# Kernel optimization log

Measured on AMD Instinct MI355X. Metric: run time of the kernel, lower is better.

Reference implementation:

```python
import jax, jax.numpy as jnp
import numpy as np

B, N, E = 32, 2048, 768
OUT = 384
SPARSITY = 4
LOCAL_C = (E + SPARSITY - 1) // SPARSITY  # 192
HID = 16
LN_EPS = 1e-5


def _layernorm(x, w, b):
    mu = jnp.mean(x, axis=-1, keepdims=True)
    var = jnp.mean(jnp.square(x - mu), axis=-1, keepdims=True)
    return (x - mu) * jax.lax.rsqrt(var + LN_EPS) * w + b


def setup_inputs() -> dict:
    key = jax.random.key(0)
    ks = jax.random.split(key, 8)
    s = 0.02
    return {
        "x": jax.random.normal(ks[0], (B, N, E), dtype=jnp.float32),
        # global head: Linear(E,16) -> LN(16) -> GELU -> Linear(16,1)
        "w_g1": jax.random.normal(ks[1], (E, HID), dtype=jnp.float32) * s,
        "b_g1": jnp.zeros((HID,), dtype=jnp.float32),
        "ln_g_w": jnp.ones((HID,), dtype=jnp.float32),
        "ln_g_b": jnp.zeros((HID,), dtype=jnp.float32),
        "w_g2": jax.random.normal(ks[2], (HID, 1), dtype=jnp.float32) * s,
        "b_g2": jnp.zeros((1,), dtype=jnp.float32),
        # local head: Linear(192,384) -> LN(384) -> GELU
        "w_l": jax.random.normal(ks[3], (LOCAL_C, OUT), dtype=jnp.float32) * s,
        "b_l": jnp.zeros((OUT,), dtype=jnp.float32),
        "ln_l_w": jnp.ones((OUT,), dtype=jnp.float32),
        "ln_l_b": jnp.zeros((OUT,), dtype=jnp.float32),
    }


def reference(x, w_g1, b_g1, ln_g_w, ln_g_b, w_g2, b_g2, w_l, b_l, ln_l_w, ln_l_b):
    # local branch: strided gather -> Linear -> LN -> GELU  [B,N,OUT]
    local = x[..., ::SPARSITY]                                   # [B,N,192]
    local_feat = jax.nn.gelu(_layernorm(local @ w_l + b_l, ln_l_w, ln_l_b),
                             approximate=False)
    # global branch: Linear -> LN -> GELU -> Linear -> [B,N,1] (broadcasts)
    g = jax.nn.gelu(_layernorm(x @ w_g1 + b_g1, ln_g_w, ln_g_b),
                    approximate=False)
    global_feat = g @ w_g2 + b_g2                                # [B,N,1]
    # AdaptiveAvgPool1d(OUT) on last dim; E % OUT == 0 -> exact pairwise mean
    pooled = jnp.mean(x.reshape(B, N, OUT, E // OUT), axis=-1)   # [B,N,OUT]
    return global_feat + pooled + local_feat
```

## Files before the change

kernel.cpp:

```cpp
#include <hip/hip_runtime.h>
#include <hip/hip_bf16.h>

#define B_   32
#define N_   2048
#define E_   768
#define OUT_ 384
#define HID_ 16
constexpr int ROWS   = B_ * N_;
constexpr int TILE_M = 32;
constexpr int NT     = OUT_ / 16;
constexpr int KT_L   = 6;
constexpr int KT_G   = 24;
constexpr int S_AL   = 194;
constexpr int S_PL   = 392;

typedef __attribute__((ext_vector_type(8))) short bf16x8;
typedef __attribute__((ext_vector_type(4))) float f32x4;

__device__ __forceinline__ short f2bf(float f) {
  __hip_bfloat16 h = __float2bfloat16(f);
  return __builtin_bit_cast(short, h);
}
__device__ __forceinline__ float bf2f(short s) {
  union { unsigned u; float f; } v; v.u = ((unsigned)(unsigned short)s) << 16;
  return v.f;
}

__device__ __forceinline__ void gload_pair(f32x4& d0, f32x4& d1, const float* a) {
  asm volatile("global_load_dwordx4 %0, %2, off\n\t"
               "global_load_dwordx4 %1, %2, off offset:16"
               : "=&v"(d0), "=&v"(d1)
               : "v"(a));
}
__device__ __forceinline__ void gload_frag(bf16x8& d, const short* a) {
  asm volatile("global_load_dwordx4 %0, %1, off" : "=&v"(d) : "v"(a));
}
#define WAITV(n) do { asm volatile("s_waitcnt vmcnt(" #n ")" ::: "memory"); \
                      __builtin_amdgcn_sched_barrier(0); } while (0)
#define RAWBAR() do { __builtin_amdgcn_sched_barrier(0);                     \
                      asm volatile("s_waitcnt lgkmcnt(0)" ::: "memory");     \
                      __builtin_amdgcn_s_barrier();                          \
                      __builtin_amdgcn_sched_barrier(0); } while (0)

__device__ __forceinline__ float fast_erf(float x) {
  const float ax = __builtin_fabsf(x);
  const float t  = __builtin_amdgcn_rcpf(__builtin_fmaf(0.47047f, ax, 1.0f));
  float p = __builtin_fmaf(0.7478556f, t, -0.0958798f);
  p = __builtin_fmaf(p, t, 0.3480242f);
  const float e = __expf(-ax * ax);
  const float y = __builtin_fmaf(-p * t, e, 1.0f);
  return __builtin_copysignf(y, x);
}
__device__ __forceinline__ float gelu(float v) {
  return 0.5f * v * (1.0f + fast_erf(v * 0.70710678118654752f));
}

__global__ void prep_kernel(const float* __restrict__ w_l, const float* __restrict__ w_g1,
                            short* __restrict__ wsL, short* __restrict__ wsG) {
  int t = blockIdx.x * blockDim.x + threadIdx.x;
  int wave = t >> 6, ln = t & 63;
  int kg = ln >> 4, c16 = ln & 15;
  if (wave < NT * KT_L) {
    int n = wave / KT_L, ks = wave % KT_L;
    bf16x8 v;
#pragma unroll
    for (int j = 0; j < 8; ++j) {
      int k = ks * 32 + kg * 8 + j;
      v[j] = f2bf(w_l[k * OUT_ + n * 16 + c16]);
    }
    *reinterpret_cast<bf16x8*>(&wsL[(size_t)(wave * 64 + ln) * 8]) = v;
  } else if (wave < NT * KT_L + KT_G) {
    int ks = wave - NT * KT_L;
    bf16x8 v;
#pragma unroll
    for (int j = 0; j < 8; ++j) {
      int k = ks * 32 + kg * 8 + j;
      v[j] = f2bf(w_g1[k * HID_ + c16]);
    }
    *reinterpret_cast<bf16x8*>(&wsG[(size_t)(ks * 64 + ln) * 8]) = v;
  }
}

template <bool USE_WS>
__global__ __launch_bounds__(256, 2)
void spectre_kernel(const float* __restrict__ x,
                    const float* __restrict__ w_g1, const float* __restrict__ b_g1,
                    const float* __restrict__ ln_g_w, const float* __restrict__ ln_g_b,
                    const float* __restrict__ w_g2, const float* __restrict__ b_g2,
                    const float* __restrict__ w_l, const float* __restrict__ b_l,
                    const float* __restrict__ ln_l_w, const float* __restrict__ ln_l_b,
                    const short* __restrict__ wsL, const short* __restrict__ wsG,
                    float* __restrict__ out) {
  __shared__ short al[TILE_M * S_AL];
  __shared__ short pl[TILE_M * S_PL];
  __shared__ float red2[4][16][17];
  __shared__ float reds[4][32][2];
  __shared__ float gfl[32];

  const int tid = threadIdx.x;
  const int wv  = tid >> 6;
  const int wvp = wv >> 1;
  const int wvk = wv & 1;
  const int ln  = tid & 63;
  const int kg  = ln >> 4;
  const int l15 = ln & 15;
  const int row0 = blockIdx.x * TILE_M;

  const float* xb = x + (size_t)(row0 + wvp * 16) * E_;

  const float bg  = b_g1[l15];
  const float lgw = ln_g_w[l15];
  const float lgb = ln_g_b[l15];
  const float wg2 = w_g2[l15];
  const float bg2 = b_g2[0];
  float blv[6], lwv[6], lbv[6];
#pragma unroll
  for (int j = 0; j < 6; ++j) {
    const int col = (wv * 6 + j) * 16 + l15;
    blv[j] = b_l[col];
    lwv[j] = ln_l_w[col];
    lbv[j] = ln_l_b[col];
  }
  const short* wlp = USE_WS ? (wsL + ((size_t)(wv * 6) * KT_L * 64 + ln) * 8) : nullptr;

  f32x4 accg = {0.f, 0.f, 0.f, 0.f};
  const int alr = (wvp * 16 + l15);
  if constexpr (USE_WS) {
    asm volatile("s_waitcnt vmcnt(0)" ::: "memory");
    __builtin_amdgcn_sched_barrier(0);

    bf16x8 gbv[12];
    const short* wgp = wsG + ((size_t)(wvk * 12) * 64 + ln) * 8;
#pragma unroll
    for (int i = 0; i < 12; ++i) gload_frag(gbv[i], wgp + i * 512);

    f32x4 xa0[6], xa1[6], xb0[6], xb1[6];
    const float* pA = xb + l15 * E_ + kg * 8;
#pragma unroll
    for (int i = 0; i < 6; ++i) gload_pair(xa0[i], xa1[i], pA + (wvk * 12 + i) * 32);
#pragma unroll
    for (int i = 0; i < 6; ++i) gload_pair(xb0[i], xb1[i], pA + (wvk * 12 + 6 + i) * 32);

    WAITV(12);
#pragma unroll
    for (int i = 0; i < 6; ++i) {
      const int ks = wvk * 12 + i;
      const f32x4 u0 = xa0[i], u1 = xa1[i];
      short2 lv;
      lv.x = f2bf(u0[0]);
      lv.y = f2bf(u1[0]);
      *reinterpret_cast<short2*>(&al[alr * S_AL + 8 * ks + 2 * kg]) = lv;
      short4 pv;
      pv.x = f2bf(0.5f * (u0[0] + u0[1]));
      pv.y = f2bf(0.5f * (u0[2] + u0[3]));
      pv.z = f2bf(0.5f * (u1[0] + u1[1]));
      pv.w = f2bf(0.5f * (u1[2] + u1[3]));
      *reinterpret_cast<short4*>(&pl[alr * S_PL + ks * 16 + kg * 4]) = pv;
      const bf16x8 a = { lv.x, f2bf(u0[1]), f2bf(u0[2]), f2bf(u0[3]),
                         lv.y, f2bf(u1[1]), f2bf(u1[2]), f2bf(u1[3]) };
      accg = __builtin_amdgcn_mfma_f32_16x16x32_bf16(a, gbv[i], accg, 0, 0, 0);
    }
    WAITV(0);
#pragma unroll
    for (int i = 0; i < 6; ++i) {
      const int ks = wvk * 12 + 6 + i;
      const f32x4 u0 = xb0[i], u1 = xb1[i];
      short2 lv;
      lv.x = f2bf(u0[0]);
      lv.y = f2bf(u1[0]);
      *reinterpret_cast<short2*>(&al[alr * S_AL + 8 * ks + 2 * kg]) = lv;
      short4 pv;
      pv.x = f2bf(0.5f * (u0[0] + u0[1]));
      pv.y = f2bf(0.5f * (u0[2] + u0[3]));
      pv.z = f2bf(0.5f * (u1[0] + u1[1]));
      pv.w = f2bf(0.5f * (u1[2] + u1[3]));
      *reinterpret_cast<short4*>(&pl[alr * S_PL + ks * 16 + kg * 4]) = pv;
      const bf16x8 a = { lv.x, f2bf(u0[1]), f2bf(u0[2]), f2bf(u0[3]),
                         lv.y, f2bf(u1[1]), f2bf(u1[2]), f2bf(u1[3]) };
      accg = __builtin_amdgcn_mfma_f32_16x16x32_bf16(a, gbv[6 + i], accg, 0, 0, 0);
    }
    __builtin_amdgcn_sched_barrier(0);
  } else {
    const float* pA = xb + l15 * E_ + kg * 8;
#pragma unroll
    for (int i = 0; i < 12; ++i) {
      const int ks = wvk * 12 + i;
      const float4 u0 = *reinterpret_cast<const float4*>(pA + ks * 32);
      const float4 u1 = *reinterpret_cast<const float4*>(pA + ks * 32 + 4);
      short2 lv;
      lv.x = f2bf(u0.x);
      lv.y = f2bf(u1.x);
      *reinterpret_cast<short2*>(&al[alr * S_AL + 8 * ks + 2 * kg]) = lv;
      short4 pv;
      pv.x = f2bf(0.5f * (u0.x + u0.y));
      pv.y = f2bf(0.5f * (u0.z + u0.w));
      pv.z = f2bf(0.5f * (u1.x + u1.y));
      pv.w = f2bf(0.5f * (u1.z + u1.w));
      *reinterpret_cast<short4*>(&pl[alr * S_PL + ks * 16 + kg * 4]) = pv;
      bf16x8 b;
#pragma unroll
      for (int j = 0; j < 8; ++j) b[j] = f2bf(w_g1[(ks * 32 + kg * 8 + j) * HID_ + l15]);
      const bf16x8 a = { lv.x, f2bf(u0.y), f2bf(u0.z), f2bf(u0.w),
                         lv.y, f2bf(u1.y), f2bf(u1.z), f2bf(u1.w) };
      accg = __builtin_amdgcn_mfma_f32_16x16x32_bf16(a, b, accg, 0, 0, 0);
    }
  }
#pragma unroll
  for (int r = 0; r < 4; ++r) red2[wv][kg * 4 + r][l15] = accg[r];

  bf16x8 fA[6], fB[6];
  if constexpr (USE_WS) {
#pragma unroll
    for (int j = 0; j < 6; ++j) gload_frag(fA[j], wlp + (j * 6 + 0) * 512);
#pragma unroll
    for (int j = 0; j < 6; ++j) gload_frag(fB[j], wlp + (j * 6 + 1) * 512);
    RAWBAR();
  } else {
    __syncthreads();
  }

  f32x4 acc0[6], acc1[6];
#pragma unroll
  for (int j = 0; j < 6; ++j) {
    acc0[j] = (f32x4){0.f, 0.f, 0.f, 0.f};
    acc1[j] = (f32x4){0.f, 0.f, 0.f, 0.f};
  }

  if constexpr (USE_WS) {
    float gf[4];
#pragma unroll
    for (int r = 0; r < 4; ++r) {
      const int row = kg * 4 + r;
      const float y = red2[2 * wvp][row][l15] + red2[2 * wvp + 1][row][l15] + bg;
      float s = y, q = y * y;
#pragma unroll
      for (int m = 1; m < 16; m <<= 1) {
        s += __shfl_xor(s, m);
        q += __shfl_xor(q, m);
      }
      const float mean = s * (1.f / 16.f);
      const float var  = q * (1.f / 16.f) - mean * mean;
      const float rstd = rsqrtf(var + 1e-5f);
      const float vn = (y - mean) * rstd * lgw + lgb;
      float ps = gelu(vn) * wg2;
#pragma unroll
      for (int m = 1; m < 16; m <<= 1) ps += __shfl_xor(ps, m);
      gf[r] = ps + bg2;
    }
    if (wvk == 0 && l15 == 0) {
#pragma unroll
      for (int r = 0; r < 4; ++r) gfl[wvp * 16 + kg * 4 + r] = gf[r];
    }

#define LKSTEP(KS, FREG, NEXTKS, NEXTREG, LASTWAIT)                                   \
    do {                                                                              \
      WAITV(LASTWAIT);                                                                \
      const bf16x8 aL0 = *reinterpret_cast<const bf16x8*>(                            \
          &al[l15 * S_AL + (KS) * 32 + kg * 8]);                                      \
      const bf16x8 aL1 = *reinterpret_cast<const bf16x8*>(                            \
          &al[(16 + l15) * S_AL + (KS) * 32 + kg * 8]);                               \
      __builtin_amdgcn_s_setprio(1);                                                  \
      _Pragma("unroll")                                                               \
      for (int j = 0; j < 6; ++j) {                                                   \
        acc0[j] = __builtin_amdgcn_mfma_f32_16x16x32_bf16(aL0, FREG[j], acc0[j], 0, 0, 0); \
        acc1[j] = __builtin_amdgcn_mfma_f32_16x16x32_bf16(aL1, FREG[j], acc1[j], 0, 0, 0); \
      }                                                                               \
      __builtin_amdgcn_s_setprio(0);                                                  \
      if ((NEXTKS) < KT_L) {                                                          \
        _Pragma("unroll")                                                             \
        for (int j = 0; j < 6; ++j)                                                   \
          gload_frag(NEXTREG[j], wlp + (j * 6 + (NEXTKS)) * 512);                     \
      }                                                                               \
    } while (0)

    LKSTEP(0, fA, 2, fA, 6);
    LKSTEP(1, fB, 3, fB, 6);
    LKSTEP(2, fA, 4, fA, 6);
    LKSTEP(3, fB, 5, fB, 6);
    LKSTEP(4, fA, 6, fA, 6);
    LKSTEP(5, fB, 6, fB, 0);
#undef LKSTEP
    __builtin_amdgcn_sched_barrier(0);
  } else {
    float gf[4];
#pragma unroll
    for (int r = 0; r < 4; ++r) {
      const int row = kg * 4 + r;
      const float y = red2[2 * wvp][row][l15] + red2[2 * wvp + 1][row][l15] + bg;
      float s = y, q = y * y;
#pragma unroll
      for (int m = 1; m < 16; m <<= 1) { s += __shfl_xor(s, m); q += __shfl_xor(q, m); }
      const float mean = s * (1.f / 16.f);
      const float var  = q * (1.f / 16.f) - mean * mean;
      const float rstd = rsqrtf(var + 1e-5f);
      const float vn = (y - mean) * rstd * lgw + lgb;
      float ps = gelu(vn) * wg2;
#pragma unroll
      for (int m = 1; m < 16; m <<= 1) ps += __shfl_xor(ps, m);
      gf[r] = ps + bg2;
    }
    if (wvk == 0 && l15 == 0) {
#pragma unroll
      for (int r = 0; r < 4; ++r) gfl[wvp * 16 + kg * 4 + r] = gf[r];
    }
#pragma unroll
    for (int ks = 0; ks < KT_L; ++ks) {
      const bf16x8 aL0 = *reinterpret_cast<const bf16x8*>(&al[l15 * S_AL + ks * 32 + kg * 8]);
      const bf16x8 aL1 = *reinterpret_cast<const bf16x8*>(&al[(16 + l15) * S_AL + ks * 32 + kg * 8]);
#pragma unroll
      for (int j = 0; j < 6; ++j) {
        const int ng = wv * 6 + j;
        bf16x8 b;
#pragma unroll
        for (int jj = 0; jj < 8; ++jj)
          b[jj] = f2bf(w_l[(ks * 32 + kg * 8 + jj) * OUT_ + ng * 16 + l15]);
        acc0[j] = __builtin_amdgcn_mfma_f32_16x16x32_bf16(aL0, b, acc0[j], 0, 0, 0);
        acc1[j] = __builtin_amdgcn_mfma_f32_16x16x32_bf16(aL1, b, acc1[j], 0, 0, 0);
      }
    }
  }

  float s10[4] = {0.f, 0.f, 0.f, 0.f}, s20[4] = {0.f, 0.f, 0.f, 0.f};
  float s11[4] = {0.f, 0.f, 0.f, 0.f}, s21[4] = {0.f, 0.f, 0.f, 0.f};
#pragma unroll
  for (int j = 0; j < 6; ++j) {
#pragma unroll
    for (int r = 0; r < 4; ++r) {
      const float v0 = acc0[j][r] + blv[j];
      acc0[j][r] = v0;
      s10[r] += v0; s20[r] += v0 * v0;
      const float v1 = acc1[j][r] + blv[j];
      acc1[j][r] = v1;
      s11[r] += v1; s21[r] += v1 * v1;
    }
  }
#pragma unroll
  for (int m = 1; m < 16; m <<= 1) {
#pragma unroll
    for (int r = 0; r < 4; ++r) {
      s10[r] += __shfl_xor(s10[r], m);
      s20[r] += __shfl_xor(s20[r], m);
      s11[r] += __shfl_xor(s11[r], m);
      s21[r] += __shfl_xor(s21[r], m);
    }
  }
  if (l15 == 0) {
#pragma unroll
    for (int r = 0; r < 4; ++r) {
      reds[wv][kg * 4 + r][0] = s10[r];
      reds[wv][kg * 4 + r][1] = s20[r];
      reds[wv][16 + kg * 4 + r][0] = s11[r];
      reds[wv][16 + kg * 4 + r][1] = s21[r];
    }
  }
  if constexpr (USE_WS) {
    RAWBAR();
  } else {
    __syncthreads();
  }

  float mean0[4], rstd0[4], mean1[4], rstd1[4];
#pragma unroll
  for (int r = 0; r < 4; ++r) {
    const int row = kg * 4 + r;
    float t1 = reds[0][row][0] + reds[1][row][0] + reds[2][row][0] + reds[3][row][0];
    float t2 = reds[0][row][1] + reds[1][row][1] + reds[2][row][1] + reds[3][row][1];
    mean0[r] = t1 * (1.f / 384.f);
    rstd0[r] = rsqrtf(t2 * (1.f / 384.f) - mean0[r] * mean0[r] + 1e-5f);
    t1 = reds[0][16 + row][0] + reds[1][16 + row][0] + reds[2][16 + row][0] + reds[3][16 + row][0];
    t2 = reds[0][16 + row][1] + reds[1][16 + row][1] + reds[2][16 + row][1] + reds[3][16 + row][1];
    mean1[r] = t1 * (1.f / 384.f);
    rstd1[r] = rsqrtf(t2 * (1.f / 384.f) - mean1[r] * mean1[r] + 1e-5f);
  }
#pragma unroll
  for (int n = 0; n < 6; ++n) {
    const int col = (wv * 6 + n) * 16 + l15;
#pragma unroll
    for (int r = 0; r < 4; ++r) {
      const int rowA = kg * 4 + r;
      {
        const float pooled = bf2f(pl[rowA * S_PL + col]);
        const float vn = (acc0[n][r] - mean0[r]) * rstd0[r] * lwv[n] + lbv[n];
        out[(size_t)(row0 + rowA) * OUT_ + col] = gelu(vn) + gfl[rowA] + pooled;
      }
      {
        const int rowB = 16 + rowA;
        const float pooled = bf2f(pl[rowB * S_PL + col]);
        const float vn = (acc1[n][r] - mean1[r]) * rstd1[r] * lwv[n] + lbv[n];
        out[(size_t)(row0 + rowB) * OUT_ + col] = gelu(vn) + gfl[rowB] + pooled;
      }
    }
  }
}

extern "C" void kernel_launch(void* const* d_in, const int* in_sizes, int n_in,
                              void* d_out, int out_size, void* d_ws, size_t ws_size,
                              hipStream_t stream) {
  (void)in_sizes; (void)n_in; (void)out_size;
  const float* x      = (const float*)d_in[0];
  const float* w_g1   = (const float*)d_in[1];
  const float* b_g1   = (const float*)d_in[2];
  const float* ln_g_w = (const float*)d_in[3];
  const float* ln_g_b = (const float*)d_in[4];
  const float* w_g2   = (const float*)d_in[5];
  const float* b_g2   = (const float*)d_in[6];
  const float* w_l    = (const float*)d_in[7];
  const float* b_l    = (const float*)d_in[8];
  const float* ln_l_w = (const float*)d_in[9];
  const float* ln_l_b = (const float*)d_in[10];
  float* out = (float*)d_out;

  const size_t needL = (size_t)NT * KT_L * 64 * 8;
  const size_t needG = (size_t)KT_G * 64 * 8;
  const bool use_ws = ws_size >= (needL + needG) * sizeof(short);

  short* wsL = (short*)d_ws;
  short* wsG = wsL + needL;

  const int grid = ROWS / TILE_M;
  if (use_ws) {
    prep_kernel<<<(NT * KT_L + KT_G) * 64 / 256, 256, 0, stream>>>(w_l, w_g1, wsL, wsG);
    spectre_kernel<true><<<grid, 256, 0, stream>>>(x, w_g1, b_g1, ln_g_w, ln_g_b, w_g2, b_g2,
                                                   w_l, b_l, ln_l_w, ln_l_b, wsL, wsG, out);
  } else {
    spectre_kernel<false><<<grid, 256, 0, stream>>>(x, w_g1, b_g1, ln_g_w, ln_g_b, w_g2, b_g2,
                                                    w_l, b_l, ln_l_w, ln_l_b, nullptr, nullptr, out);
  }
}
```

Before: 87.51 us.

## Cut register footprint to double occupancy with ring-buffered streaming loads

Raises the launch-bounds occupancy target from 2 to 4 blocks per CU and restructures the global-head and local-head loops to use smaller rotating register buffers. x is streamed through a 4-slot ring, and local weight fragments go through 3 half-width buffers with finer-grained waits. The LayerNorm weight and bias loads move to after the reduction barrier. The aim is to fit in fewer VGPRs so more waves can hide memory latency, at the risk of spills or shallower per-wave prefetch.

```diff
diff --git a/kernel.cpp b/kernel.cpp
--- a/kernel.cpp
+++ b/kernel.cpp
@@ -82,7 +82,7 @@
 }
 
 template <bool USE_WS>
-__global__ __launch_bounds__(256, 2)
+__global__ __launch_bounds__(256, 4)
 void spectre_kernel(const float* __restrict__ x,
                     const float* __restrict__ w_g1, const float* __restrict__ b_g1,
                     const float* __restrict__ ln_g_w, const float* __restrict__ ln_g_b,
@@ -113,72 +113,53 @@
   const float lgb = ln_g_b[l15];
   const float wg2 = w_g2[l15];
   const float bg2 = b_g2[0];
-  float blv[6], lwv[6], lbv[6];
-#pragma unroll
-  for (int j = 0; j < 6; ++j) {
-    const int col = (wv * 6 + j) * 16 + l15;
-    blv[j] = b_l[col];
-    lwv[j] = ln_l_w[col];
-    lbv[j] = ln_l_b[col];
-  }
+  float blv[6];
+#pragma unroll
+  for (int j = 0; j < 6; ++j) blv[j] = b_l[(wv * 6 + j) * 16 + l15];
   const short* wlp = USE_WS ? (wsL + ((size_t)(wv * 6) * KT_L * 64 + ln) * 8) : nullptr;
 
   f32x4 accg = {0.f, 0.f, 0.f, 0.f};
   const int alr = (wvp * 16 + l15);
   if constexpr (USE_WS) {
+    bf16x8 gbv[12];
+#pragma unroll
+    for (int i = 0; i < 12; ++i)
+      gbv[i] = *reinterpret_cast<const bf16x8*>(&wsG[((wvk * 12 + i) * 64 + ln) * 8]);
+
     asm volatile("s_waitcnt vmcnt(0)" ::: "memory");
     __builtin_amdgcn_sched_barrier(0);
 
-    bf16x8 gbv[12];
-    const short* wgp = wsG + ((size_t)(wvk * 12) * 64 + ln) * 8;
-#pragma unroll
-    for (int i = 0; i < 12; ++i) gload_frag(gbv[i], wgp + i * 512);
-
-    f32x4 xa0[6], xa1[6], xb0[6], xb1[6];
+    f32x4 x0[4], x1[4];
     const float* pA = xb + l15 * E_ + kg * 8;
 #pragma unroll
-    for (int i = 0; i < 6; ++i) gload_pair(xa0[i], xa1[i], pA + (wvk * 12 + i) * 32);
-#pragma unroll
-    for (int i = 0; i < 6; ++i) gload_pair(xb0[i], xb1[i], pA + (wvk * 12 + 6 + i) * 32);
-
-    WAITV(12);
-#pragma unroll
-    for (int i = 0; i < 6; ++i) {
-      const int ks = wvk * 12 + i;
-      const f32x4 u0 = xa0[i], u1 = xa1[i];
-      short2 lv;
-      lv.x = f2bf(u0[0]);
-      lv.y = f2bf(u1[0]);
-      *reinterpret_cast<short2*>(&al[alr * S_AL + 8 * ks + 2 * kg]) = lv;
-      short4 pv;
-      pv.x = f2bf(0.5f * (u0[0] + u0[1]));
-      pv.y = f2bf(0.5f * (u0[2] + u0[3]));
-      pv.z = f2bf(0.5f * (u1[0] + u1[1]));
-      pv.w = f2bf(0.5f * (u1[2] + u1[3]));
-      *reinterpret_cast<short4*>(&pl[alr * S_PL + ks * 16 + kg * 4]) = pv;
-      const bf16x8 a = { lv.x, f2bf(u0[1]), f2bf(u0[2]), f2bf(u0[3]),
-                         lv.y, f2bf(u1[1]), f2bf(u1[2]), f2bf(u1[3]) };
-      accg = __builtin_amdgcn_mfma_f32_16x16x32_bf16(a, gbv[i], accg, 0, 0, 0);
-    }
-    WAITV(0);
-#pragma unroll
-    for (int i = 0; i < 6; ++i) {
-      const int ks = wvk * 12 + 6 + i;
-      const f32x4 u0 = xb0[i], u1 = xb1[i];
-      short2 lv;
-      lv.x = f2bf(u0[0]);
-      lv.y = f2bf(u1[0]);
-      *reinterpret_cast<short2*>(&al[alr * S_AL + 8 * ks + 2 * kg]) = lv;
-      short4 pv;
-      pv.x = f2bf(0.5f * (u0[0] + u0[1]));
-      pv.y = f2bf(0.5f * (u0[2] + u0[3]));
-      pv.z = f2bf(0.5f * (u1[0] + u1[1]));
-      pv.w = f2bf(0.5f * (u1[2] + u1[3]));
-      *reinterpret_cast<short4*>(&pl[alr * S_PL + ks * 16 + kg * 4]) = pv;
-      const bf16x8 a = { lv.x, f2bf(u0[1]), f2bf(u0[2]), f2bf(u0[3]),
-                         lv.y, f2bf(u1[1]), f2bf(u1[2]), f2bf(u1[3]) };
-      accg = __builtin_amdgcn_mfma_f32_16x16x32_bf16(a, gbv[6 + i], accg, 0, 0, 0);
-    }
+    for (int s = 0; s < 4; ++s) gload_pair(x0[s], x1[s], pA + (wvk * 12 + s) * 32);
+
+#define GSTEP(I, SLOT, WAIT)                                                          \
+    do {                                                                              \
+      WAITV(WAIT);                                                                    \
+      const int ks = wvk * 12 + (I);                                                  \
+      const f32x4 u0 = x0[SLOT], u1 = x1[SLOT];                                       \
+      short2 lv;                                                                      \
+      lv.x = f2bf(u0[0]);                                                             \
+      lv.y = f2bf(u1[0]);                                                             \
+      *reinterpret_cast<short2*>(&al[alr * S_AL + 8 * ks + 2 * kg]) = lv;             \
+      short4 pv;                                                                      \
+      pv.x = f2bf(0.5f * (u0[0] + u0[1]));                                            \
+      pv.y = f2bf(0.5f * (u0[2] + u0[3]));                                            \
+      pv.z = f2bf(0.5f * (u1[0] + u1[1]));                                            \
+      pv.w = f2bf(0.5f * (u1[2] + u1[3]));                                            \
+      *reinterpret_cast<short4*>(&pl[alr * S_PL + ks * 16 + kg * 4]) = pv;            \
+      const bf16x8 a = { lv.x, f2bf(u0[1]), f2bf(u0[2]), f2bf(u0[3]),                 \
+                         lv.y, f2bf(u1[1]), f2bf(u1[2]), f2bf(u1[3]) };               \
+      accg = __builtin_amdgcn_mfma_f32_16x16x32_bf16(a, gbv[I], accg, 0, 0, 0);       \
+      if ((I) + 4 < 12)                                                               \
+        gload_pair(x0[SLOT], x1[SLOT], pA + (wvk * 12 + (I) + 4) * 32);               \
+    } while (0)
+
+    GSTEP(0, 0, 6);  GSTEP(1, 1, 6);  GSTEP(2, 2, 6);  GSTEP(3, 3, 6);
+    GSTEP(4, 0, 6);  GSTEP(5, 1, 6);  GSTEP(6, 2, 6);  GSTEP(7, 3, 6);
+    GSTEP(8, 0, 6);  GSTEP(9, 1, 4);  GSTEP(10, 2, 2); GSTEP(11, 3, 0);
+#undef GSTEP
     __builtin_amdgcn_sched_barrier(0);
   } else {
     const float* pA = xb + l15 * E_ + kg * 8;
@@ -208,12 +189,14 @@
 #pragma unroll
   for (int r = 0; r < 4; ++r) red2[wv][kg * 4 + r][l15] = accg[r];
 
-  bf16x8 fA[6], fB[6];
+  bf16x8 fb0[3], fb1[3], fb2[3];
   if constexpr (USE_WS) {
 #pragma unroll
-    for (int j = 0; j < 6; ++j) gload_frag(fA[j], wlp + (j * 6 + 0) * 512);
-#pragma unroll
-    for (int j = 0; j < 6; ++j) gload_frag(fB[j], wlp + (j * 6 + 1) * 512);
+    for (int j = 0; j < 3; ++j) gload_frag(fb0[j], wlp + ((0 + j) * 6 + 0) * 512);
+#pragma unroll
+    for (int j = 0; j < 3; ++j) gload_frag(fb1[j], wlp + ((3 + j) * 6 + 0) * 512);
+#pragma unroll
+    for (int j = 0; j < 3; ++j) gload_frag(fb2[j], wlp + ((0 + j) * 6 + 1) * 512);
     RAWBAR();
   } else {
     __syncthreads();
@@ -252,34 +235,37 @@
       for (int r = 0; r < 4; ++r) gfl[wvp * 16 + kg * 4 + r] = gf[r];
     }
 
-#define LKSTEP(KS, FREG, NEXTKS, NEXTREG, LASTWAIT)                                   \
+    bf16x8 aL0, aL1;
+#define LSTEP(K, BUF, WAIT)                                                           \
     do {                                                                              \
-      WAITV(LASTWAIT);                                                                \
-      const bf16x8 aL0 = *reinterpret_cast<const bf16x8*>(                            \
-          &al[l15 * S_AL + (KS) * 32 + kg * 8]);                                      \
-      const bf16x8 aL1 = *reinterpret_cast<const bf16x8*>(                            \
-          &al[(16 + l15) * S_AL + (KS) * 32 + kg * 8]);                               \
+      WAITV(WAIT);                                                                    \
+      if (((K) & 1) == 0) {                                                           \
+        aL0 = *reinterpret_cast<const bf16x8*>(                                       \
+            &al[l15 * S_AL + ((K) >> 1) * 32 + kg * 8]);                              \
+        aL1 = *reinterpret_cast<const bf16x8*>(                                       \
+            &al[(16 + l15) * S_AL + ((K) >> 1) * 32 + kg * 8]);                       \
+      }                                                                               \
       __builtin_amdgcn_s_setprio(1);                                                  \
       _Pragma("unroll")                                                               \
-      for (int j = 0; j < 6; ++j) {                                                   \
-        acc0[j] = __builtin_amdgcn_mfma_f32_16x16x32_bf16(aL0, FREG[j], acc0[j], 0, 0, 0); \
-        acc1[j] = __builtin_amdgcn_mfma_f32_16x16x32_bf16(aL1, FREG[j], acc1[j], 0, 0, 0); \
+      for (int j = 0; j < 3; ++j) {                                                   \
+        const int n = 3 * ((K) & 1) + j;                                              \
+        acc0[n] = __builtin_amdgcn_mfma_f32_16x16x32_bf16(aL0, BUF[j], acc0[n], 0, 0, 0); \
+        acc1[n] = __builtin_amdgcn_mfma_f32_16x16x32_bf16(aL1, BUF[j], acc1[n], 0, 0, 0); \
       }                                                                               \
       __builtin_amdgcn_s_setprio(0);                                                  \
-      if ((NEXTKS) < KT_L) {                                                          \
+      if ((K) + 3 < 12) {                                                             \
         _Pragma("unroll")                                                             \
-        for (int j = 0; j < 6; ++j)                                                   \
-          gload_frag(NEXTREG[j], wlp + (j * 6 + (NEXTKS)) * 512);                     \
+        for (int j = 0; j < 3; ++j)                                                   \
+          gload_frag(BUF[j],                                                          \
+              wlp + ((3 * (((K) + 3) & 1) + j) * 6 + (((K) + 3) >> 1)) * 512);        \
       }                                                                               \
     } while (0)
 
-    LKSTEP(0, fA, 2, fA, 6);
-    LKSTEP(1, fB, 3, fB, 6);
-    LKSTEP(2, fA, 4, fA, 6);
-    LKSTEP(3, fB, 5, fB, 6);
-    LKSTEP(4, fA, 6, fA, 6);
-    LKSTEP(5, fB, 6, fB, 0);
-#undef LKSTEP
+    LSTEP(0,  fb0, 6);  LSTEP(1,  fb1, 6);  LSTEP(2,  fb2, 6);
+    LSTEP(3,  fb0, 6);  LSTEP(4,  fb1, 6);  LSTEP(5,  fb2, 6);
+    LSTEP(6,  fb0, 6);  LSTEP(7,  fb1, 6);  LSTEP(8,  fb2, 6);
+    LSTEP(9,  fb0, 6);  LSTEP(10, fb1, 3);  LSTEP(11, fb2, 0);
+#undef LSTEP
     __builtin_amdgcn_sched_barrier(0);
   } else {
     float gf[4];
@@ -357,6 +343,14 @@
     RAWBAR();
   } else {
     __syncthreads();
+  }
+
+  float lwv[6], lbv[6];
+#pragma unroll
+  for (int j = 0; j < 6; ++j) {
+    const int col = (wv * 6 + j) * 16 + l15;
+    lwv[j] = ln_l_w[col];
+    lbv[j] = ln_l_b[col];
   }
 
   float mean0[4], rstd0[4], mean1[4], rstd1[4];
```

New measurement: 89.21 us. About the same (+1.9%).
